# Kernel optimization log

Hardware: AMD Instinct MI355X
Metric: run time of the kernel (lower is better)

Reference implementation:

```python
import jax, jax.numpy as jnp
import numpy as np

B = 65536
S_IN = 256     # n_scalars_in (256x0e)
S_OUT = 128    # n_scalars_out (128x0e)
MUL = 32       # multiplicity of 1o and 2e irreps
COND = 64
D1, D2 = 3, 5  # dims of l=1, l=2 irreps
WNUM = MUL * MUL * 2  # per-sample weight_numel = 2048


def setup_inputs() -> dict:
    key = jax.random.key(0)
    ks = jax.random.split(key, 9)
    scale = lambda d: 1.0 / np.sqrt(d)
    return {
        "features": jax.random.normal(ks[0], (B, S_IN + MUL * (D1 + D2)), jnp.float32),
        "conditioning_tensor": jax.random.normal(ks[1], (B, COND), jnp.float32),
        # FiLM 1: cond -> (gamma, beta) for scalars
        "film1_w": jax.random.normal(ks[2], (COND, 2 * S_IN), jnp.float32) * scale(COND),
        "film1_b": jnp.zeros((2 * S_IN,), jnp.float32),
        # fc1: scalar MLP (single linear, nequip-style no bias)
        "fc1_w": jax.random.normal(ks[3], (S_IN, S_IN), jnp.float32) * scale(S_IN),
        # FiLM 2
        "film2_w": jax.random.normal(ks[4], (COND, 2 * S_IN), jnp.float32) * scale(COND),
        "film2_b": jnp.zeros((2 * S_IN,), jnp.float32),
        # invariant readout: scalars -> S_OUT
        "inv_w": jax.random.normal(ks[5], (S_IN, S_OUT), jnp.float32) * scale(S_IN),
        # hypernetwork: scalars -> per-sample equivariant linear weights
        "wemb_w": jax.random.normal(ks[6], (S_IN, WNUM), jnp.float32) * scale(S_IN),
    }


def reference(features, conditioning_tensor, film1_w, film1_b, fc1_w,
              film2_w, film2_b, inv_w, wemb_w):
    # split scalars / equivariant parts
    scalars = features[:, :S_IN]                      # [B, 256]
    equiv = features[:, S_IN:]                        # [B, 256] flat (32x1o + 32x2e)

    # FiLM1 -> fc1 -> FiLM2 conditioning chain on scalars
    gb1 = conditioning_tensor @ film1_w + film1_b
    scalars = scalars * gb1[:, :S_IN] + gb1[:, S_IN:]
    scalars = scalars @ fc1_w
    gb2 = conditioning_tensor @ film2_w + film2_b
    scalars = scalars * gb2[:, :S_IN] + gb2[:, S_IN:]

    # invariant readout
    out_scalars = scalars @ inv_w                     # [B, 128]

    # reshape_in: flat -> [B, mul, 2l+1] per irrep
    x1 = equiv[:, : MUL * D1].reshape(B, MUL, D1)     # 1o block
    x2 = equiv[:, MUL * D1:].reshape(B, MUL, D2)      # 2e block

    # hypernet-generated per-sample weights (non-shared Linear)
    w = scalars @ wemb_w                              # [B, 2048]
    w1 = w[:, : MUL * MUL].reshape(B, MUL, MUL)
    w2 = w[:, MUL * MUL:].reshape(B, MUL, MUL)

    norm = 1.0 / np.sqrt(MUL)                         # e3nn fan-in normalization
    y1 = jnp.einsum('bio,bid->bod', w1, x1) * norm    # [B, 32, 3]
    y2 = jnp.einsum('bio,bid->bod', w2, x2) * norm    # [B, 32, 5]

    # reshape_back to flat irreps layout and concat with scalar output
    out_equiv = jnp.concatenate(
        [y1.reshape(B, MUL * D1), y2.reshape(B, MUL * D2)], axis=-1)
    return jnp.concatenate([out_scalars, out_equiv], axis=-1)  # [B, 384]
```

## Files before the change

kernel.cpp:

```cpp
#include <hip/hip_runtime.h>
#include <hip/hip_bf16.h>
#include <stdint.h>

#define BTOT 65536
#define KAUG 320
#define NBIG 2176
#define NBIG_PAD 2304
#define OUTD 384

typedef __attribute__((ext_vector_type(8))) short s16x8;
typedef __attribute__((ext_vector_type(4))) float f32x4;
typedef __attribute__((ext_vector_type(4))) uint32_t u32x4;

#define WS_WGT   0u
#define WS_WFC   (64u*1024u)
#define WS_WBIG  (224u*1024u)
#define WS_C1    (1664u*1024u)
#define WS_C2    (1665u*1024u)
#define WS_ACT   (2u*1024u*1024u)

__device__ __forceinline__ float bs2f(short s) {
    uint32_t u = ((uint32_t)(uint16_t)s) << 16; float f; __builtin_memcpy(&f, &u, 4); return f;
}
__device__ __forceinline__ short f2bs(float f) {
    __hip_bfloat16 h = __float2bfloat16(f); short s; __builtin_memcpy(&s, &h, 2); return s;
}
__device__ __forceinline__ uint32_t swz(uint32_t row, uint32_t kb) { return kb ^ ((row & 7u) << 4); }

__device__ __forceinline__ f32x4 mfma16(s16x8 a, s16x8 b, f32x4 c) {
    asm volatile("v_mfma_f32_16x16x32_bf16 %0, %1, %2, %0" : "+v"(c) : "v"(a), "v"(b));
    return c;
}

template <int NI>
__device__ __forceinline__ void issueB_t(const char* src, int tid, int base_n, int kc, u32x4 (&P)[NI]) {
#pragma unroll
    for (int i = 0; i < NI; ++i) {
        int gid = tid + i * 512; int row = gid >> 3, g = gid & 7;
        P[i] = *(const u32x4*)(src + (size_t)(base_n + row) * 640 + kc * 128 + g * 16);
    }
}
template <int NI>
__device__ __forceinline__ void commitB_t(char* dst, int tid, const u32x4 (&P)[NI]) {
#pragma unroll
    for (int i = 0; i < NI; ++i) {
        int gid = tid + i * 512; int row = gid >> 3, g = gid & 7;
        *(u32x4*)(dst + row * 128 + swz(row, g * 16)) = P[i];
    }
}

__global__ __launch_bounds__(256) void k0a(const float* __restrict__ f1w, const float* __restrict__ f2w, char* ws) {
    int idx = blockIdx.x * 256 + threadIdx.x;
    int n = idx >> 6, k = idx & 63;
    float v = (n < 256) ? f1w[k * 512 + n] : f2w[k * 512 + (n - 256)];
    ((short*)(ws + WS_WGT))[n * 64 + k] = f2bs(v);
}

__global__ __launch_bounds__(256) void k0b(const float* __restrict__ f1w, const float* __restrict__ f1b,
                                           const float* __restrict__ fc1, char* ws) {
    __shared__ float awt[256][65];
    __shared__ float fcc[256][16];
    const int tid = threadIdx.x;
    const int n0 = blockIdx.x * 16;
#pragma unroll 4
    for (int i = 0; i < 64; ++i) awt[tid][i] = f1w[i * 512 + 256 + tid];
#pragma unroll 4
    for (int i = 0; i < 16; ++i) {
        int idx = tid + i * 256; int j = idx >> 4, nl = idx & 15;
        fcc[j][nl] = fc1[j * 256 + n0 + nl];
    }
    __syncthreads();
    const int nl = tid & 15, rg = tid >> 4;
    float a0 = 0.f, a1v = 0.f, a2v = 0.f, a3v = 0.f;
    for (int j = 0; j < 256; ++j) {
        float wv = fcc[j][nl];
        a0 += awt[j][rg * 4 + 0] * wv; a1v += awt[j][rg * 4 + 1] * wv;
        a2v += awt[j][rg * 4 + 2] * wv; a3v += awt[j][rg * 4 + 3] * wv;
    }
    short* wfcT = (short*)(ws + WS_WFC);
    const int n = n0 + nl;
    wfcT[n * 320 + 256 + rg * 4 + 0] = f2bs(a0);
    wfcT[n * 320 + 256 + rg * 4 + 1] = f2bs(a1v);
    wfcT[n * 320 + 256 + rg * 4 + 2] = f2bs(a2v);
    wfcT[n * 320 + 256 + rg * 4 + 3] = f2bs(a3v);
#pragma unroll
    for (int p = 0; p < 16; ++p) { int k = rg * 16 + p; wfcT[n * 320 + k] = f2bs(fcc[k][nl]); }
    if (rg == 0) {
        float s = 0.f;
        for (int j = 0; j < 256; ++j) s += f1b[256 + j] * fcc[j][nl];
        ((float*)(ws + WS_C1))[n] = s;
    }
}

__global__ __launch_bounds__(256) void k0c(const float* __restrict__ f2w, const float* __restrict__ f2b,
                                           const float* __restrict__ invw, const float* __restrict__ wemb, char* ws) {
    __shared__ float awt[256][65];
    __shared__ float wbc[256][16];
    const int tid = threadIdx.x;
    short* wbT = (short*)(ws + WS_WBIG);
    if (blockIdx.x == 136) {
        for (int i = 0; i < 160; ++i) wbT[2176 * 320 + tid + i * 256] = 0;
        if (tid < 128) ((float*)(ws + WS_C2))[2176 + tid] = 0.f;
        return;
    }
    const int n0 = blockIdx.x * 16;
#pragma unroll 4
    for (int i = 0; i < 64; ++i) awt[tid][i] = f2w[i * 512 + 256 + tid];
#pragma unroll 4
    for (int i = 0; i < 16; ++i) {
        int idx = tid + i * 256; int j = idx >> 4, nl = idx & 15; int n = n0 + nl;
        wbc[j][nl] = (n < 128) ? invw[j * 128 + n] : wemb[j * 2048 + (n - 128)];
    }
    __syncthreads();
    const int nl = tid & 15, rg = tid >> 4;
    float a0 = 0.f, a1v = 0.f, a2v = 0.f, a3v = 0.f;
    for (int j = 0; j < 256; ++j) {
        float wv = wbc[j][nl];
        a0 += awt[j][rg * 4 + 0] * wv; a1v += awt[j][rg * 4 + 1] * wv;
        a2v += awt[j][rg * 4 + 2] * wv; a3v += awt[j][rg * 4 + 3] * wv;
    }
    const int n = n0 + nl;
    wbT[n * 320 + 256 + rg * 4 + 0] = f2bs(a0);
    wbT[n * 320 + 256 + rg * 4 + 1] = f2bs(a1v);
    wbT[n * 320 + 256 + rg * 4 + 2] = f2bs(a2v);
    wbT[n * 320 + 256 + rg * 4 + 3] = f2bs(a3v);
#pragma unroll
    for (int p = 0; p < 16; ++p) { int k = rg * 16 + p; wbT[n * 320 + k] = f2bs(wbc[k][nl]); }
    if (rg == 0) {
        float s = 0.f;
        for (int j = 0; j < 256; ++j) s += f2b[256 + j] * wbc[j][nl];
        ((float*)(ws + WS_C2))[n] = s;
    }
}

__global__ __launch_bounds__(512) void af(const float* __restrict__ feat, const float* __restrict__ cond,
                                          const float* __restrict__ f1b, const float* __restrict__ f2b, char* ws) {
    __shared__ short sCond[64 * 64];
    __shared__ short sT[64 * 256];
    __shared__ short sG2[64 * 256];
    __shared__ short sBuf[2][256 * 64];
    const int tid = threadIdx.x;
    const int r0 = blockIdx.x * 64;
    short* actw = (short*)(ws + WS_ACT);
    const char* wfc = ws + WS_WFC;

    u32x4 pfA[4], pfB[4];
    issueB_t(wfc, tid, 0, 0, pfA);
    issueB_t(wfc, tid, 0, 1, pfB);

    {
        int row = tid >> 3, g = tid & 7;
        const float* src = cond + (size_t)(r0 + row) * 64 + g * 8;
        s16x8 p;
#pragma unroll
        for (int j = 0; j < 8; ++j) p[j] = f2bs(src[j]);
        *(s16x8*)((char*)sCond + row * 128 + swz(row, g * 16)) = p;
        *(s16x8*)(actw + (size_t)(r0 + row) * 320 + 256 + g * 8) = p;
    }
    {
        const char* wgt = ws + WS_WGT;
        char* sWg = (char*)sBuf;
#pragma unroll
        for (int i = 0; i < 8; ++i) {
            int gid = tid + i * 512; int row = gid >> 3, g = gid & 7;
            u32x4 v = *(const u32x4*)(wgt + row * 128 + g * 16);
            *(u32x4*)(sWg + row * 128 + swz(row, g * 16)) = v;
        }
    }
    __syncthreads();

    const int w = tid >> 6, l = tid & 63, lr = l & 15, lk = l >> 4;
    s16x8 caf[4][2];
#pragma unroll
    for (int fm = 0; fm < 4; ++fm)
#pragma unroll
        for (int ks = 0; ks < 2; ++ks) {
            int row = fm * 16 + lr; uint32_t kb = (ks * 32 + lk * 8) * 2;
            caf[fm][ks] = *(const s16x8*)((char*)sCond + row * 128 + swz(row, kb));
        }
    {
        const char* sWg = (const char*)sBuf;
        const int nw = w * 64;
        f32x4 acc[4][4] = {};
        __builtin_amdgcn_s_setprio(1);
#pragma unroll
        for (int ks = 0; ks < 2; ++ks) {
            uint32_t kb = (ks * 32 + lk * 8) * 2;
            s16x8 bf[4];
#pragma unroll
            for (int fn = 0; fn < 4; ++fn) { int row = nw + fn * 16 + lr;
                bf[fn] = *(const s16x8*)(sWg + row * 128 + swz(row, kb)); }
#pragma unroll
            for (int fm = 0; fm < 4; ++fm)
#pragma unroll
                for (int fn = 0; fn < 4; ++fn)
                    acc[fm][fn] = mfma16(caf[fm][ks], bf[fn], acc[fm][fn]);
        }
        __builtin_amdgcn_s_setprio(0);
        asm volatile("s_nop 7\n\ts_nop 7");
        if (nw < 256) {
#pragma unroll
            for (int fm = 0; fm < 4; ++fm)
#pragma unroll
                for (int fn = 0; fn < 4; ++fn) {
                    int c = nw + fn * 16 + lr;
                    float bias = f1b[c];
#pragma unroll
                    for (int ri = 0; ri < 4; ++ri) {
                        int row = fm * 16 + lk * 4 + ri;
                        float g1 = acc[fm][fn][ri] + bias;
                        float t = feat[(size_t)(r0 + row) * 512 + c] * g1;
                        *(short*)((char*)sT + row * 512 + (((uint32_t)(c * 2)) ^ ((row & 7u) << 4))) = f2bs(t);
                    }
                }
        } else {
#pragma unroll
            for (int fm = 0; fm < 4; ++fm)
#pragma unroll
                for (int fn = 0; fn < 4; ++fn) {
                    int cg = nw - 256 + fn * 16 + lr;
                    float bias = f2b[cg];
#pragma unroll
                    for (int ri = 0; ri < 4; ++ri) {
                        int row = fm * 16 + lk * 4 + ri;
                        *(short*)((char*)sG2 + row * 512 + (((uint32_t)(cg * 2)) ^ ((row & 7u) << 4))) = f2bs(acc[fm][fn][ri] + bias);
                    }
                }
        }
    }
    __syncthreads();
    commitB_t((char*)sBuf[0], tid, pfA);
    issueB_t(wfc, tid, 0, 2, pfA);
    __syncthreads();

    const int wm = w >> 2, wn = w & 3;
    f32x4 acc2[2][4] = {};
    for (int kc = 0; kc < 5; ++kc) {
        const int pr = (kc + 1) & 1;
        if (kc <= 3) { if (pr == 0) commitB_t((char*)sBuf[0], tid, pfA); else commitB_t((char*)sBuf[1], tid, pfB); }
        if (kc <= 1) { if (pr == 0) issueB_t(wfc, tid, 0, kc + 3, pfA); else issueB_t(wfc, tid, 0, kc + 3, pfB); }
        const char* bbuf = (const char*)sBuf[kc & 1];
        __builtin_amdgcn_s_setprio(1);
#pragma unroll
        for (int ks = 0; ks < 2; ++ks) {
            uint32_t kb = (ks * 32 + lk * 8) * 2;
            s16x8 a2f[2], b2f[4];
#pragma unroll
            for (int fm = 0; fm < 2; ++fm) {
                int row = wm * 32 + fm * 16 + lr;
                if (kc < 4) a2f[fm] = *(const s16x8*)((char*)sT + row * 512 + swz(row, kc * 128 + kb));
                else        a2f[fm] = caf[wm * 2 + fm][ks];
            }
#pragma unroll
            for (int fn = 0; fn < 4; ++fn) { int row = wn * 64 + fn * 16 + lr;
                b2f[fn] = *(const s16x8*)(bbuf + row * 128 + swz(row, kb)); }
#pragma unroll
            for (int fm = 0; fm < 2; ++fm)
#pragma unroll
                for (int fn = 0; fn < 4; ++fn)
                    acc2[fm][fn] = mfma16(a2f[fm], b2f[fn], acc2[fm][fn]);
        }
        __builtin_amdgcn_s_setprio(0);
        __syncthreads();
    }
    asm volatile("s_nop 7\n\ts_nop 7");
    const float* c1 = (const float*)(ws + WS_C1);
#pragma unroll
    for (int fm = 0; fm < 2; ++fm)
#pragma unroll
        for (int fn = 0; fn < 4; ++fn) {
            int c = wn * 64 + fn * 16 + lr;
            float cc1 = c1[c];
#pragma unroll
            for (int ri = 0; ri < 4; ++ri) {
                int row = wm * 32 + fm * 16 + lk * 4 + ri;
                float s = acc2[fm][fn][ri] + cc1;
                float g2v = bs2f(*(const short*)((char*)sG2 + row * 512 + (((uint32_t)(c * 2)) ^ ((row & 7u) << 4))));
                actw[(size_t)(r0 + row) * 320 + c] = f2bs(s * g2v);
            }
        }
}

__global__ __launch_bounds__(512) void kb(const float* __restrict__ feat, char* ws, float* __restrict__ out) {
    __shared__ short sA[64 * 320];
    __shared__ short sB[2][256 * 64];
    __shared__ short sW[64 * 256];
    const int tid = threadIdx.x;
    const int r0 = blockIdx.x * 64;
    const short* actw = (const short*)(ws + WS_ACT);
    const char* wbig = ws + WS_WBIG;
    const float* c2 = (const float*)(ws + WS_C2);

    const int er = tid >> 3, slot = tid & 7;
    const int region = (slot < 3) ? 1 : 2;
    const int d = (slot < 3) ? slot : slot - 3;
    float y[32];
    float x[32];
    {
        const float* xb = feat + (size_t)(r0 + er) * 512 + 256 + ((region == 1) ? 0 : 96);
        const int stride = (region == 1) ? 3 : 5;
#pragma unroll
        for (int i = 0; i < 32; ++i) x[i] = xb[i * stride + d];
#pragma unroll
        for (int o = 0; o < 32; ++o) y[o] = 0.f;
    }

    u32x4 pfA[4], pfB[4];
    issueB_t(wbig, tid, 0, 0, pfA);
    issueB_t(wbig, tid, 0, 1, pfB);
#pragma unroll
    for (int i = 0; i < 5; ++i) {
        int gid = tid + i * 512; int row = gid / 40, g = gid % 40;
        u32x4 v = *(const u32x4*)(actw + (size_t)(r0 + row) * 320 + g * 8);
        *(u32x4*)((char*)sA + row * 640 + swz(row, g * 16)) = v;
    }
    commitB_t((char*)sB[0], tid, pfA);
    issueB_t(wbig, tid, 0, 2, pfA);
    __syncthreads();

    const int w = tid >> 6, l = tid & 63, lr = l & 15, lk = l >> 4;
    const int wm = w >> 2, wn = w & 3;
    const float norm = 0.17677669529663687f;

    int ntI = 0, kcI = 3;
    for (int nt = 0; nt < 9; ++nt) {
        const int n0 = nt * 256;
        f32x4 acc[2][4] = {};
        for (int kc = 0; kc < 5; ++kc) {
            const int q = nt * 5 + kc;
            const int pr = (q + 1) & 1;
            if (q <= 43) { if (pr == 0) commitB_t((char*)sB[0], tid, pfA); else commitB_t((char*)sB[1], tid, pfB); }
            if (q <= 41) {
                if (pr == 0) issueB_t(wbig, tid, ntI * 256, kcI, pfA); else issueB_t(wbig, tid, ntI * 256, kcI, pfB);
                if (++kcI == 5) { kcI = 0; ++ntI; }
            }
            const char* bbuf = (const char*)sB[q & 1];
            __builtin_amdgcn_s_setprio(1);
#pragma unroll
            for (int ks = 0; ks < 2; ++ks) {
                uint32_t kb = (ks * 32 + lk * 8) * 2;
                s16x8 afr[2], bf[4];
#pragma unroll
                for (int fm = 0; fm < 2; ++fm) { int row = wm * 32 + fm * 16 + lr;
                    afr[fm] = *(const s16x8*)((char*)sA + row * 640 + swz(row, kc * 128 + kb)); }
#pragma unroll
                for (int fn = 0; fn < 4; ++fn) { int row = wn * 64 + fn * 16 + lr;
                    bf[fn] = *(const s16x8*)(bbuf + row * 128 + swz(row, kb)); }
#pragma unroll
                for (int fm = 0; fm < 2; ++fm)
#pragma unroll
                    for (int fn = 0; fn < 4; ++fn)
                        acc[fm][fn] = mfma16(afr[fm], bf[fn], acc[fm][fn]);
            }
            __builtin_amdgcn_s_setprio(0);
            __syncthreads();
        }
        asm volatile("s_nop 7\n\ts_nop 7");
#pragma unroll
        for (int fm = 0; fm < 2; ++fm)
#pragma unroll
            for (int fn = 0; fn < 4; ++fn) {
                int c = n0 + wn * 64 + fn * 16 + lr;
                float cc2 = c2[c];
#pragma unroll
                for (int ri = 0; ri < 4; ++ri) {
                    int rl = wm * 32 + fm * 16 + lk * 4 + ri;
                    float v = acc[fm][fn][ri] + cc2;
                    if (c < 128) out[(size_t)(r0 + rl) * OUTD + c] = v;
                    else if (c < NBIG) {
                        int cl = wn * 64 + fn * 16 + lr;
                        *(short*)((char*)sW + rl * 512 + ((uint32_t)(cl * 2) ^ ((rl & 7u) << 4))) = f2bs(v);
                    }
                }
            }
        __syncthreads();
        for (int islot = 0; islot < 8; ++islot) {
            int cb = n0 + islot * 32;
            if (cb < 128 || cb >= NBIG) continue;
            int treg = (cb < 1152) ? 1 : 2;
            if (treg != region) continue;
            int i = (cb - ((treg == 1) ? 128 : 1152)) >> 5;
            float xv = x[i];
#pragma unroll
            for (int og = 0; og < 4; ++og) {
                uint32_t clb = (uint32_t)(islot * 64 + og * 16);
                s16x8 wv = *(const s16x8*)((const char*)sW + er * 512 + (clb ^ ((er & 7u) << 4)));
#pragma unroll
                for (int j = 0; j < 8; ++j) y[og * 8 + j] += bs2f(wv[j]) * xv;
            }
        }
        __syncthreads();
    }
    float* orow = out + (size_t)(r0 + er) * OUTD;
    if (region == 1) { for (int o = 0; o < 32; ++o) orow[128 + o * 3 + d] = y[o] * norm; }
    else             { for (int o = 0; o < 32; ++o) orow[224 + o * 5 + d] = y[o] * norm; }
}

extern "C" void kernel_launch(void* const* d_in, const int* in_sizes, int n_in,
                              void* d_out, int out_size, void* d_ws, size_t ws_size,
                              hipStream_t stream) {
    (void)in_sizes; (void)n_in; (void)out_size; (void)ws_size;
    const float* feat = (const float*)d_in[0];
    const float* cond = (const float*)d_in[1];
    const float* f1w  = (const float*)d_in[2];
    const float* f1b  = (const float*)d_in[3];
    const float* fc1  = (const float*)d_in[4];
    const float* f2w  = (const float*)d_in[5];
    const float* f2b  = (const float*)d_in[6];
    const float* invw = (const float*)d_in[7];
    const float* wemb = (const float*)d_in[8];
    char* ws = (char*)d_ws;
    float* out = (float*)d_out;

    k0a<<<128, 256, 0, stream>>>(f1w, f2w, ws);
    k0b<<<16, 256, 0, stream>>>(f1w, f1b, fc1, ws);
    k0c<<<137, 256, 0, stream>>>(f2w, f2b, invw, wemb, ws);
    af<<<1024, 512, 0, stream>>>(feat, cond, f1b, f2b, ws);
    kb<<<1024, 512, 0, stream>>>(feat, ws, out);
}
```

Before: 678.3 us.

## Load GEMM fragments straight from global into registers, dropping LDS staging

In both the FiLM kernel and the big hypernet GEMM kernel, B-operand weight fragments are now read from global memory directly into MFMA register fragments. They are double-buffered in registers instead of being committed to swizzled LDS with a barrier per K-chunk. The A operand in kb is held entirely in registers, and x features are staged in LDS rather than per-thread arrays. Launch bounds request two blocks per SU. The change removes per-chunk LDS writes and syncthreads, at the cost of more register pressure and redundant global/L2 reads of weights across waves.

```diff
diff --git a/kernel.cpp b/kernel.cpp
--- a/kernel.cpp
+++ b/kernel.cpp
@@ -2,10 +2,7 @@
 #include <hip/hip_bf16.h>
 #include <stdint.h>
 
-#define BTOT 65536
-#define KAUG 320
 #define NBIG 2176
-#define NBIG_PAD 2304
 #define OUTD 384
 
 typedef __attribute__((ext_vector_type(8))) short s16x8;
@@ -30,23 +27,6 @@
 __device__ __forceinline__ f32x4 mfma16(s16x8 a, s16x8 b, f32x4 c) {
     asm volatile("v_mfma_f32_16x16x32_bf16 %0, %1, %2, %0" : "+v"(c) : "v"(a), "v"(b));
     return c;
-}
-
-template <int NI>
-__device__ __forceinline__ void issueB_t(const char* src, int tid, int base_n, int kc, u32x4 (&P)[NI]) {
-#pragma unroll
-    for (int i = 0; i < NI; ++i) {
-        int gid = tid + i * 512; int row = gid >> 3, g = gid & 7;
-        P[i] = *(const u32x4*)(src + (size_t)(base_n + row) * 640 + kc * 128 + g * 16);
-    }
-}
-template <int NI>
-__device__ __forceinline__ void commitB_t(char* dst, int tid, const u32x4 (&P)[NI]) {
-#pragma unroll
-    for (int i = 0; i < NI; ++i) {
-        int gid = tid + i * 512; int row = gid >> 3, g = gid & 7;
-        *(u32x4*)(dst + row * 128 + swz(row, g * 16)) = P[i];
-    }
 }
 
 __global__ __launch_bounds__(256) void k0a(const float* __restrict__ f1w, const float* __restrict__ f2w, char* ws) {
@@ -133,136 +113,113 @@
     }
 }
 
-__global__ __launch_bounds__(512) void af(const float* __restrict__ feat, const float* __restrict__ cond,
-                                          const float* __restrict__ f1b, const float* __restrict__ f2b, char* ws) {
-    __shared__ short sCond[64 * 64];
-    __shared__ short sT[64 * 256];
-    __shared__ short sG2[64 * 256];
-    __shared__ short sBuf[2][256 * 64];
+__global__ __launch_bounds__(512, 2) void af(const float* __restrict__ feat, const float* __restrict__ cond,
+                                             const float* __restrict__ f1b, const float* __restrict__ f2b, char* ws) {
+    __shared__ char sm[65536];
+    char* sT = sm; char* sG2 = sm + 32768;
     const int tid = threadIdx.x;
     const int r0 = blockIdx.x * 64;
     short* actw = (short*)(ws + WS_ACT);
     const char* wfc = ws + WS_WFC;
-
-    u32x4 pfA[4], pfB[4];
-    issueB_t(wfc, tid, 0, 0, pfA);
-    issueB_t(wfc, tid, 0, 1, pfB);
-
+    const char* wgt = ws + WS_WGT;
+    const int w = tid >> 6, l = tid & 63, lr = l & 15, lk = l >> 4;
+    const int wm = w >> 2, wn = w & 3;
+
+    s16x8 F0[8], F1[8];
+#define AF_ISSUE(BUF, KC) do { \
+    const char* bp_ = wfc + (size_t)(wn * 64 + lr) * 640 + ((KC) * 64 + lk * 8) * 2; \
+    _Pragma("unroll") for (int fn_ = 0; fn_ < 4; ++fn_) \
+    _Pragma("unroll") for (int ks_ = 0; ks_ < 2; ++ks_) \
+        BUF[fn_ * 2 + ks_] = *(const s16x8*)(bp_ + fn_ * (16 * 640) + ks_ * 64); } while (0)
+
+    s16x8 caf[4][2];
+#pragma unroll
+    for (int fm = 0; fm < 4; ++fm)
+#pragma unroll
+        for (int ks = 0; ks < 2; ++ks) {
+            const float* cp = cond + (size_t)(r0 + fm * 16 + lr) * 64 + ks * 32 + lk * 8;
+            f32x4 c0 = *(const f32x4*)cp, c1 = *(const f32x4*)(cp + 4);
+            s16x8 p;
+#pragma unroll
+            for (int j = 0; j < 4; ++j) { p[j] = f2bs(c0[j]); p[4 + j] = f2bs(c1[j]); }
+            caf[fm][ks] = p;
+        }
     {
         int row = tid >> 3, g = tid & 7;
         const float* src = cond + (size_t)(r0 + row) * 64 + g * 8;
         s16x8 p;
 #pragma unroll
         for (int j = 0; j < 8; ++j) p[j] = f2bs(src[j]);
-        *(s16x8*)((char*)sCond + row * 128 + swz(row, g * 16)) = p;
         *(s16x8*)(actw + (size_t)(r0 + row) * 320 + 256 + g * 8) = p;
     }
-    {
-        const char* wgt = ws + WS_WGT;
-        char* sWg = (char*)sBuf;
-#pragma unroll
-        for (int i = 0; i < 8; ++i) {
-            int gid = tid + i * 512; int row = gid >> 3, g = gid & 7;
-            u32x4 v = *(const u32x4*)(wgt + row * 128 + g * 16);
-            *(u32x4*)(sWg + row * 128 + swz(row, g * 16)) = v;
-        }
+    s16x8 wgf[4][2];
+#pragma unroll
+    for (int fn = 0; fn < 4; ++fn)
+#pragma unroll
+        for (int ks = 0; ks < 2; ++ks)
+            wgf[fn][ks] = *(const s16x8*)(wgt + (size_t)(w * 64 + fn * 16 + lr) * 128 + (ks * 32 + lk * 8) * 2);
+
+    const int nw = w * 64;
+    f32x4 acc[4][4] = {};
+#pragma unroll
+    for (int ks = 0; ks < 2; ++ks)
+#pragma unroll
+        for (int fm = 0; fm < 4; ++fm)
+#pragma unroll
+            for (int fn = 0; fn < 4; ++fn)
+                acc[fm][fn] = mfma16(caf[fm][ks], wgf[fn][ks], acc[fm][fn]);
+    asm volatile("s_nop 7\n\ts_nop 7");
+
+    AF_ISSUE(F0, 0);
+    AF_ISSUE(F1, 1);
+
+    if (nw < 256) {
+#pragma unroll
+        for (int fm = 0; fm < 4; ++fm)
+#pragma unroll
+            for (int fn = 0; fn < 4; ++fn) {
+                int c = nw + fn * 16 + lr;
+                float bias = f1b[c];
+#pragma unroll
+                for (int ri = 0; ri < 4; ++ri) {
+                    int row = fm * 16 + lk * 4 + ri;
+                    float g1 = acc[fm][fn][ri] + bias;
+                    float t = feat[(size_t)(r0 + row) * 512 + c] * g1;
+                    *(short*)(sT + row * 512 + (((uint32_t)(c * 2)) ^ ((row & 7u) << 4))) = f2bs(t);
+                }
+            }
+    } else {
+#pragma unroll
+        for (int fm = 0; fm < 4; ++fm)
+#pragma unroll
+            for (int fn = 0; fn < 4; ++fn) {
+                int cg = nw - 256 + fn * 16 + lr;
+                float bias = f2b[cg];
+#pragma unroll
+                for (int ri = 0; ri < 4; ++ri) {
+                    int row = fm * 16 + lk * 4 + ri;
+                    *(short*)(sG2 + row * 512 + (((uint32_t)(cg * 2)) ^ ((row & 7u) << 4))) = f2bs(acc[fm][fn][ri] + bias);
+                }
+            }
     }
     __syncthreads();
 
-    const int w = tid >> 6, l = tid & 63, lr = l & 15, lk = l >> 4;
-    s16x8 caf[4][2];
-#pragma unroll
-    for (int fm = 0; fm < 4; ++fm)
-#pragma unroll
-        for (int ks = 0; ks < 2; ++ks) {
-            int row = fm * 16 + lr; uint32_t kb = (ks * 32 + lk * 8) * 2;
-            caf[fm][ks] = *(const s16x8*)((char*)sCond + row * 128 + swz(row, kb));
-        }
-    {
-        const char* sWg = (const char*)sBuf;
-        const int nw = w * 64;
-        f32x4 acc[4][4] = {};
-        __builtin_amdgcn_s_setprio(1);
-#pragma unroll
-        for (int ks = 0; ks < 2; ++ks) {
-            uint32_t kb = (ks * 32 + lk * 8) * 2;
-            s16x8 bf[4];
-#pragma unroll
-            for (int fn = 0; fn < 4; ++fn) { int row = nw + fn * 16 + lr;
-                bf[fn] = *(const s16x8*)(sWg + row * 128 + swz(row, kb)); }
-#pragma unroll
-            for (int fm = 0; fm < 4; ++fm)
-#pragma unroll
-                for (int fn = 0; fn < 4; ++fn)
-                    acc[fm][fn] = mfma16(caf[fm][ks], bf[fn], acc[fm][fn]);
-        }
-        __builtin_amdgcn_s_setprio(0);
-        asm volatile("s_nop 7\n\ts_nop 7");
-        if (nw < 256) {
-#pragma unroll
-            for (int fm = 0; fm < 4; ++fm)
-#pragma unroll
-                for (int fn = 0; fn < 4; ++fn) {
-                    int c = nw + fn * 16 + lr;
-                    float bias = f1b[c];
-#pragma unroll
-                    for (int ri = 0; ri < 4; ++ri) {
-                        int row = fm * 16 + lk * 4 + ri;
-                        float g1 = acc[fm][fn][ri] + bias;
-                        float t = feat[(size_t)(r0 + row) * 512 + c] * g1;
-                        *(short*)((char*)sT + row * 512 + (((uint32_t)(c * 2)) ^ ((row & 7u) << 4))) = f2bs(t);
-                    }
-                }
-        } else {
-#pragma unroll
-            for (int fm = 0; fm < 4; ++fm)
-#pragma unroll
-                for (int fn = 0; fn < 4; ++fn) {
-                    int cg = nw - 256 + fn * 16 + lr;
-                    float bias = f2b[cg];
-#pragma unroll
-                    for (int ri = 0; ri < 4; ++ri) {
-                        int row = fm * 16 + lk * 4 + ri;
-                        *(short*)((char*)sG2 + row * 512 + (((uint32_t)(cg * 2)) ^ ((row & 7u) << 4))) = f2bs(acc[fm][fn][ri] + bias);
-                    }
-                }
-        }
-    }
-    __syncthreads();
-    commitB_t((char*)sBuf[0], tid, pfA);
-    issueB_t(wfc, tid, 0, 2, pfA);
-    __syncthreads();
-
-    const int wm = w >> 2, wn = w & 3;
     f32x4 acc2[2][4] = {};
-    for (int kc = 0; kc < 5; ++kc) {
-        const int pr = (kc + 1) & 1;
-        if (kc <= 3) { if (pr == 0) commitB_t((char*)sBuf[0], tid, pfA); else commitB_t((char*)sBuf[1], tid, pfB); }
-        if (kc <= 1) { if (pr == 0) issueB_t(wfc, tid, 0, kc + 3, pfA); else issueB_t(wfc, tid, 0, kc + 3, pfB); }
-        const char* bbuf = (const char*)sBuf[kc & 1];
-        __builtin_amdgcn_s_setprio(1);
-#pragma unroll
-        for (int ks = 0; ks < 2; ++ks) {
-            uint32_t kb = (ks * 32 + lk * 8) * 2;
-            s16x8 a2f[2], b2f[4];
-#pragma unroll
-            for (int fm = 0; fm < 2; ++fm) {
-                int row = wm * 32 + fm * 16 + lr;
-                if (kc < 4) a2f[fm] = *(const s16x8*)((char*)sT + row * 512 + swz(row, kc * 128 + kb));
-                else        a2f[fm] = caf[wm * 2 + fm][ks];
-            }
-#pragma unroll
-            for (int fn = 0; fn < 4; ++fn) { int row = wn * 64 + fn * 16 + lr;
-                b2f[fn] = *(const s16x8*)(bbuf + row * 128 + swz(row, kb)); }
-#pragma unroll
-            for (int fm = 0; fm < 2; ++fm)
-#pragma unroll
-                for (int fn = 0; fn < 4; ++fn)
-                    acc2[fm][fn] = mfma16(a2f[fm], b2f[fn], acc2[fm][fn]);
-        }
-        __builtin_amdgcn_s_setprio(0);
-        __syncthreads();
-    }
+#define AF_CHUNK(BUF, KC) do { \
+    _Pragma("unroll") for (int ks = 0; ks < 2; ++ks) { \
+        uint32_t kb_ = (ks * 32 + lk * 8) * 2; \
+        s16x8 a2f[2]; \
+        _Pragma("unroll") for (int fm = 0; fm < 2; ++fm) { \
+            int row = wm * 32 + fm * 16 + lr; \
+            if ((KC) < 4) a2f[fm] = *(const s16x8*)(sT + row * 512 + swz(row, (KC) * 128 + kb_)); \
+            else          a2f[fm] = caf[wm * 2 + fm][ks]; } \
+        _Pragma("unroll") for (int fm = 0; fm < 2; ++fm) \
+        _Pragma("unroll") for (int fn = 0; fn < 4; ++fn) \
+            acc2[fm][fn] = mfma16(a2f[fm], BUF[fn * 2 + ks], acc2[fm][fn]); } \
+    if ((KC) + 2 <= 4) AF_ISSUE(BUF, (KC) + 2); } while (0)
+
+    AF_CHUNK(F0, 0); AF_CHUNK(F1, 1); AF_CHUNK(F0, 2); AF_CHUNK(F1, 3); AF_CHUNK(F0, 4);
+
     asm volatile("s_nop 7\n\ts_nop 7");
     const float* c1 = (const float*)(ws + WS_C1);
 #pragma unroll
@@ -275,86 +232,80 @@
             for (int ri = 0; ri < 4; ++ri) {
                 int row = wm * 32 + fm * 16 + lk * 4 + ri;
                 float s = acc2[fm][fn][ri] + cc1;
-                float g2v = bs2f(*(const short*)((char*)sG2 + row * 512 + (((uint32_t)(c * 2)) ^ ((row & 7u) << 4))));
+                float g2v = bs2f(*(const short*)(sG2 + row * 512 + (((uint32_t)(c * 2)) ^ ((row & 7u) << 4))));
                 actw[(size_t)(r0 + row) * 320 + c] = f2bs(s * g2v);
             }
         }
-}
-
-__global__ __launch_bounds__(512) void kb(const float* __restrict__ feat, char* ws, float* __restrict__ out) {
-    __shared__ short sA[64 * 320];
-    __shared__ short sB[2][256 * 64];
-    __shared__ short sW[64 * 256];
+#undef AF_CHUNK
+#undef AF_ISSUE
+}
+
+__global__ __launch_bounds__(512, 2) void kb(const float* __restrict__ feat, char* ws, float* __restrict__ out) {
+    __shared__ char sm[98304];
+    char* sWm = sm; char* sXm = sm + 32768;
     const int tid = threadIdx.x;
     const int r0 = blockIdx.x * 64;
-    const short* actw = (const short*)(ws + WS_ACT);
+    const char* actb = ws + WS_ACT;
     const char* wbig = ws + WS_WBIG;
     const float* c2 = (const float*)(ws + WS_C2);
+    const int w = tid >> 6, l = tid & 63, lr = l & 15, lk = l >> 4;
+    const int wm = w >> 2, wn = w & 3;
+
+    s16x8 B0[8], B1[8];
+    int ntI = 0, kcI = 0, qNext = 0;
+    auto issue = [&](s16x8 (&B)[8]) {
+        if (qNext <= 44) {
+            const char* bp = wbig + (size_t)(ntI * 256 + wn * 64 + lr) * 640 + (kcI * 64 + lk * 8) * 2;
+#pragma unroll
+            for (int fn = 0; fn < 4; ++fn)
+#pragma unroll
+                for (int ks = 0; ks < 2; ++ks)
+                    B[fn * 2 + ks] = *(const s16x8*)(bp + fn * (16 * 640) + ks * 64);
+            ++qNext; if (++kcI == 5) { kcI = 0; ++ntI; }
+        }
+    };
+    issue(B0); issue(B1);
+
+    {
+        int row = tid >> 3, seg = tid & 7;
+        const float* src = feat + (size_t)(r0 + row) * 512 + 256 + seg * 32;
+#pragma unroll
+        for (int q = 0; q < 8; ++q) {
+            f32x4 v = *(const f32x4*)(src + q * 4);
+            *(f32x4*)(sXm + row * 1024 + ((uint32_t)(seg * 128 + q * 16) ^ ((row & 7u) << 4))) = v;
+        }
+    }
+    s16x8 Afr[2][10];
+#pragma unroll
+    for (int fm = 0; fm < 2; ++fm)
+#pragma unroll
+        for (int ki = 0; ki < 10; ++ki)
+            Afr[fm][ki] = *(const s16x8*)(actb + (size_t)(r0 + wm * 32 + fm * 16 + lr) * 640 + (ki * 32 + lk * 8) * 2);
 
     const int er = tid >> 3, slot = tid & 7;
     const int region = (slot < 3) ? 1 : 2;
     const int d = (slot < 3) ? slot : slot - 3;
     float y[32];
-    float x[32];
-    {
-        const float* xb = feat + (size_t)(r0 + er) * 512 + 256 + ((region == 1) ? 0 : 96);
-        const int stride = (region == 1) ? 3 : 5;
-#pragma unroll
-        for (int i = 0; i < 32; ++i) x[i] = xb[i * stride + d];
-#pragma unroll
-        for (int o = 0; o < 32; ++o) y[o] = 0.f;
-    }
-
-    u32x4 pfA[4], pfB[4];
-    issueB_t(wbig, tid, 0, 0, pfA);
-    issueB_t(wbig, tid, 0, 1, pfB);
-#pragma unroll
-    for (int i = 0; i < 5; ++i) {
-        int gid = tid + i * 512; int row = gid / 40, g = gid % 40;
-        u32x4 v = *(const u32x4*)(actw + (size_t)(r0 + row) * 320 + g * 8);
-        *(u32x4*)((char*)sA + row * 640 + swz(row, g * 16)) = v;
-    }
-    commitB_t((char*)sB[0], tid, pfA);
-    issueB_t(wbig, tid, 0, 2, pfA);
-    __syncthreads();
-
-    const int w = tid >> 6, l = tid & 63, lr = l & 15, lk = l >> 4;
-    const int wm = w >> 2, wn = w & 3;
+#pragma unroll
+    for (int o = 0; o < 32; ++o) y[o] = 0.f;
     const float norm = 0.17677669529663687f;
 
-    int ntI = 0, kcI = 3;
+    f32x4 acc[2][4];
+#define KB_CHUNK(BUF, KC) do { \
+    _Pragma("unroll") for (int ks = 0; ks < 2; ++ks) \
+    _Pragma("unroll") for (int fm = 0; fm < 2; ++fm) \
+    _Pragma("unroll") for (int fn = 0; fn < 4; ++fn) \
+        acc[fm][fn] = mfma16(Afr[fm][(KC) * 2 + ks], BUF[fn * 2 + ks], acc[fm][fn]); \
+    issue(BUF); } while (0)
+
     for (int nt = 0; nt < 9; ++nt) {
         const int n0 = nt * 256;
-        f32x4 acc[2][4] = {};
-        for (int kc = 0; kc < 5; ++kc) {
-            const int q = nt * 5 + kc;
-            const int pr = (q + 1) & 1;
-            if (q <= 43) { if (pr == 0) commitB_t((char*)sB[0], tid, pfA); else commitB_t((char*)sB[1], tid, pfB); }
-            if (q <= 41) {
-                if (pr == 0) issueB_t(wbig, tid, ntI * 256, kcI, pfA); else issueB_t(wbig, tid, ntI * 256, kcI, pfB);
-                if (++kcI == 5) { kcI = 0; ++ntI; }
-            }
-            const char* bbuf = (const char*)sB[q & 1];
-            __builtin_amdgcn_s_setprio(1);
-#pragma unroll
-            for (int ks = 0; ks < 2; ++ks) {
-                uint32_t kb = (ks * 32 + lk * 8) * 2;
-                s16x8 afr[2], bf[4];
-#pragma unroll
-                for (int fm = 0; fm < 2; ++fm) { int row = wm * 32 + fm * 16 + lr;
-                    afr[fm] = *(const s16x8*)((char*)sA + row * 640 + swz(row, kc * 128 + kb)); }
-#pragma unroll
-                for (int fn = 0; fn < 4; ++fn) { int row = wn * 64 + fn * 16 + lr;
-                    bf[fn] = *(const s16x8*)(bbuf + row * 128 + swz(row, kb)); }
-#pragma unroll
-                for (int fm = 0; fm < 2; ++fm)
-#pragma unroll
-                    for (int fn = 0; fn < 4; ++fn)
-                        acc[fm][fn] = mfma16(afr[fm], bf[fn], acc[fm][fn]);
-            }
-            __builtin_amdgcn_s_setprio(0);
-            __syncthreads();
-        }
+#pragma unroll
+        for (int fm = 0; fm < 2; ++fm)
+#pragma unroll
+            for (int fn = 0; fn < 4; ++fn) acc[fm][fn] = f32x4{0.f, 0.f, 0.f, 0.f};
+        if (!(nt & 1)) { KB_CHUNK(B0, 0); KB_CHUNK(B1, 1); KB_CHUNK(B0, 2); KB_CHUNK(B1, 3); KB_CHUNK(B0, 4); }
+        else           { KB_CHUNK(B1, 0); KB_CHUNK(B0, 1); KB_CHUNK(B1, 2); KB_CHUNK(B0, 3); KB_CHUNK(B1, 4); }
         asm volatile("s_nop 7\n\ts_nop 7");
 #pragma unroll
         for (int fm = 0; fm < 2; ++fm)
@@ -369,7 +320,7 @@
                     if (c < 128) out[(size_t)(r0 + rl) * OUTD + c] = v;
                     else if (c < NBIG) {
                         int cl = wn * 64 + fn * 16 + lr;
-                        *(short*)((char*)sW + rl * 512 + ((uint32_t)(cl * 2) ^ ((rl & 7u) << 4))) = f2bs(v);
+                        *(short*)(sWm + rl * 512 + ((uint32_t)(cl * 2) ^ ((rl & 7u) << 4))) = f2bs(v);
                     }
                 }
             }
@@ -380,20 +331,27 @@
             int treg = (cb < 1152) ? 1 : 2;
             if (treg != region) continue;
             int i = (cb - ((treg == 1) ? 128 : 1152)) >> 5;
-            float xv = x[i];
+            int xcol = ((treg == 1) ? 0 : 96) + i * ((treg == 1) ? 3 : 5) + d;
+            float xv = *(const float*)(sXm + er * 1024 + ((uint32_t)(xcol * 4) ^ ((er & 7u) << 4)));
 #pragma unroll
             for (int og = 0; og < 4; ++og) {
                 uint32_t clb = (uint32_t)(islot * 64 + og * 16);
-                s16x8 wv = *(const s16x8*)((const char*)sW + er * 512 + (clb ^ ((er & 7u) << 4)));
+                s16x8 wv = *(const s16x8*)(sWm + er * 512 + (clb ^ ((er & 7u) << 4)));
 #pragma unroll
                 for (int j = 0; j < 8; ++j) y[og * 8 + j] += bs2f(wv[j]) * xv;
             }
         }
         __syncthreads();
     }
+#undef KB_CHUNK
     float* orow = out + (size_t)(r0 + er) * OUTD;
-    if (region == 1) { for (int o = 0; o < 32; ++o) orow[128 + o * 3 + d] = y[o] * norm; }
-    else             { for (int o = 0; o < 32; ++o) orow[224 + o * 5 + d] = y[o] * norm; }
+    if (region == 1) {
+#pragma unroll
+        for (int o = 0; o < 32; ++o) orow[128 + o * 3 + d] = y[o] * norm;
+    } else {
+#pragma unroll
+        for (int o = 0; o < 32; ++o) orow[224 + o * 5 + d] = y[o] * norm;
+    }
 }
 
 extern "C" void kernel_launch(void* const* d_in, const int* in_sizes, int n_in,
```

Result: slower. 1.314 ms (+93.7%).
